# Kernel tuning notes

Measured on AMD Instinct MI355X. Metric: run time of the kernel, lower is better.

Reference implementation:

```python
import jax, jax.numpy as jnp
import numpy as np

N_NODES = 100000


def _deg_norm(idx, n):
    # inverse-sqrt degree, zero-degree nodes -> 0 (DGL norm='both' convention)
    deg = jax.ops.segment_sum(jnp.ones(idx.shape, jnp.float32), idx, num_segments=n)
    return jnp.where(deg > 0, jax.lax.rsqrt(jnp.maximum(deg, 1.0)), 0.0)


def graph_conv(x, src, dst, W, b, n):
    # symmetric normalization: D_out^{-1/2} on src, D_in^{-1/2} on dst
    norm_src = _deg_norm(src, n)  # [N]
    norm_dst = _deg_norm(dst, n)  # [N]
    h = (x * norm_src[:, None]) @ W          # apply weight first (in >= out)
    msg = h[src]                              # gather [E, out]
    agg = jax.ops.segment_sum(msg, dst, num_segments=n)  # scatter-add [N, out]
    return agg * norm_dst[:, None] + b


def setup_inputs() -> dict:
    key = jax.random.key(0)
    ks = jax.random.split(key, 6)
    x = jax.random.normal(ks[0], (N_NODES, 128), dtype=jnp.float32)
    edge_index = jax.random.randint(ks[1], (2, 1600000), 0, N_NODES, dtype=jnp.int64)
    W1 = jax.random.normal(ks[2], (128, 64), dtype=jnp.float32) * (1.0 / np.sqrt(128))
    b1 = jnp.zeros((64,), jnp.float32)
    W2 = jax.random.normal(ks[3], (64, 32), dtype=jnp.float32) * (1.0 / np.sqrt(64))
    b2 = jnp.zeros((32,), jnp.float32)
    Wl = jax.random.normal(ks[4], (32, 1), dtype=jnp.float32) * (1.0 / np.sqrt(32))
    bl = jnp.zeros((1,), jnp.float32)
    return {"x": x, "edge_index": edge_index, "W1": W1, "b1": b1,
            "W2": W2, "b2": b2, "Wl": Wl, "bl": bl}


def reference(x, edge_index, W1, b1, W2, b2, Wl, bl):
    src, dst = edge_index[0], edge_index[1]
    n = x.shape[0]
    h = graph_conv(x, src, dst, W1, b1, n)
    h = jax.nn.relu(h)
    # dropout(p=0.5) is identity at inference
    h = graph_conv(h, src, dst, W2, b2, n)
    return h @ Wl + bl  # [N, 1]
```

## Files before the change

### kernel.cpp

```cpp
#include <hip/hip_runtime.h>
#include <hip/hip_fp16.h>


#define WAVE 64
#define NRANGE 8
#define NQUAD 2
#define CB 1024

typedef _Float16 f16x8 __attribute__((ext_vector_type(8)));
typedef float f32x4 __attribute__((ext_vector_type(4)));

__global__ __launch_bounds__(256) void k_hist(const int* __restrict__ srcArr,
                                              const int* __restrict__ dstArr,
                                              unsigned* __restrict__ partial_s,
                                              unsigned* __restrict__ partial_d,
                                              int E, int B, int C, int chunkE) {
    extern __shared__ unsigned hist[];
    const int q = blockIdx.x & (NQUAD - 1);
    const int c = blockIdx.x >> 1;
    const int lo = q * 4 * B;
    const int* nodes = blockIdx.y ? dstArr : srcArr;
    unsigned* partial = blockIdx.y ? partial_d : partial_s;

    for (int b = threadIdx.x; b < B; b += 256) hist[b] = 0u;
    __syncthreads();

    const int beg = c * chunkE, end = min(beg + chunkE, E);
    const int n4 = (end - beg) >> 2;
    const int4* p = (const int4*)(nodes + beg);
    for (int j = threadIdx.x; j < n4; j += 256) {
        int4 v = p[j];
#pragma unroll
        for (int k = 0; k < 4; ++k) {
            int a = (&v.x)[k] - lo;
            if ((unsigned)a < (unsigned)(4 * B)) {
                int h2 = (a >= 2 * B);
                int r2 = a - (h2 ? 2 * B : 0);
                int h1 = (r2 >= B);
                int bin = r2 - (h1 ? B : 0);
                atomicAdd(&hist[bin], 1u << (((h2 << 1) | h1) << 3));
            }
        }
    }
    for (int j = beg + (n4 << 2) + threadIdx.x; j < end; j += 256) {
        int a = nodes[j] - lo;
        if ((unsigned)a < (unsigned)(4 * B)) {
            int h2 = (a >= 2 * B);
            int r2 = a - (h2 ? 2 * B : 0);
            int h1 = (r2 >= B);
            int bin = r2 - (h1 ? B : 0);
            atomicAdd(&hist[bin], 1u << (((h2 << 1) | h1) << 3));
        }
    }
    __syncthreads();
    unsigned* outp = partial + (size_t)(q * C + c) * B;
    for (int b = threadIdx.x; b < B; b += 256) outp[b] = hist[b];
}

__global__ __launch_bounds__(256) void k_reduce_norm(const unsigned* __restrict__ partial_s,
                                                     unsigned* __restrict__ partial_d,
                                                     float* __restrict__ norm_s,
                                                     float* __restrict__ norm_d,
                                                     unsigned* __restrict__ deg_d,
                                                     int N, int B, int C) {
    int t = blockIdx.x * 256 + threadIdx.x;
    if (t >= NQUAD * B) return;
    int q = t / B, b = t - q * B;
    size_t base = (size_t)(q * C) * B + b;
    unsigned ds = 0;
    for (int c = 0; c < C; ++c) ds += partial_s[base + (size_t)c * B];
    unsigned run = 0;
    for (int c = 0; c < C; ++c) {
        size_t ix = base + (size_t)c * B;
        unsigned v = partial_d[ix];
        partial_d[ix] = run;
        run += v;
    }
#pragma unroll
    for (int j = 0; j < 4; ++j) {
        int n = q * 4 * B + j * B + b;
        if (n < N) {
            unsigned d0 = (ds >> (8 * j)) & 0xffu;
            unsigned d1 = (run >> (8 * j)) & 0xffu;
            deg_d[n] = d1;
            norm_s[n] = d0 ? rsqrtf((float)d0) : 0.0f;
            norm_d[n] = d1 ? rsqrtf((float)d1) : 0.0f;
        }
    }
}

__global__ __launch_bounds__(256) void k_prep(const float* __restrict__ W1,
                                              const float* __restrict__ W2,
                                              const float* __restrict__ b2,
                                              const float* __restrict__ Wl,
                                              const float* __restrict__ bl,
                                              _Float16* __restrict__ wt,
                                              float* __restrict__ w2l,
                                              float* __restrict__ c0) {
    int t = threadIdx.x;
    for (int i = 0; i < 32; ++i) {
        int e = i * 256 + t;
        int k = e >> 6, n = e & 63;
        wt[n * 128 + k] = (_Float16)W1[e];
    }
    if (t < 64) {
        float acc = 0.f;
#pragma unroll
        for (int j = 0; j < 32; ++j) acc += W2[t * 32 + j] * Wl[j];
        w2l[t] = acc;
    }
    if (t == 0) {
        float s = 0.f;
#pragma unroll
        for (int j = 0; j < 32; ++j) s += b2[j] * Wl[j];
        *c0 = s + bl[0];
    }
}

__global__ __launch_bounds__(256) void k_blocksum(const unsigned* __restrict__ deg,
                                                  unsigned* __restrict__ partial, int N) {
    __shared__ unsigned sw[4];
    int i = blockIdx.x * 256 + threadIdx.x;
    unsigned v = (i < N) ? deg[i] : 0u;
#pragma unroll
    for (int off = 32; off; off >>= 1) v += __shfl_xor((int)v, off);
    if ((threadIdx.x & 63) == 0) sw[threadIdx.x >> 6] = v;
    __syncthreads();
    if (threadIdx.x == 0) partial[blockIdx.x] = sw[0] + sw[1] + sw[2] + sw[3];
}

__global__ __launch_bounds__(512) void k_scanpartial(const unsigned* __restrict__ partial,
                                                     unsigned* __restrict__ blockoff,
                                                     unsigned* __restrict__ offsets,
                                                     int nb, int N) {
    __shared__ unsigned s[512];
    int t = threadIdx.x;
    unsigned v = (t < nb) ? partial[t] : 0u;
    s[t] = v;
    __syncthreads();
    for (int off = 1; off < 512; off <<= 1) {
        unsigned a = (t >= off) ? s[t - off] : 0u;
        __syncthreads();
        s[t] += a;
        __syncthreads();
    }
    if (t < nb) blockoff[t] = s[t] - v;
    if (t == nb - 1) offsets[N] = s[t];
}

__global__ __launch_bounds__(256) void k_offsets(const unsigned* __restrict__ deg,
                                                 const unsigned* __restrict__ blockoff,
                                                 unsigned* __restrict__ offsets, int N) {
    __shared__ unsigned s[256];
    int t = threadIdx.x;
    int i = blockIdx.x * 256 + t;
    unsigned v = (i < N) ? deg[i] : 0u;
    s[t] = v;
    __syncthreads();
    for (int off = 1; off < 256; off <<= 1) {
        unsigned a = (t >= off) ? s[t - off] : 0u;
        __syncthreads();
        s[t] += a;
        __syncthreads();
    }
    if (i < N) offsets[i] = blockoff[blockIdx.x] + s[t] - v;
}

__global__ __launch_bounds__(256) void k_cnt(const int* __restrict__ dst,
                                             unsigned* __restrict__ cnt,
                                             int E, int B, int chunkEb) {
    __shared__ unsigned lc[NRANGE];
    if (threadIdx.x < NRANGE) lc[threadIdx.x] = 0u;
    __syncthreads();
    const int c = blockIdx.x;
    const int beg = c * chunkEb, end = min(beg + chunkEb, E);
    unsigned pc[NRANGE] = {};
    for (int i = beg + (int)threadIdx.x; i < end; i += 256) {
        int r = dst[i] / B;
#pragma unroll
        for (int rr = 0; rr < NRANGE; ++rr) pc[rr] += (r == rr);
    }
#pragma unroll
    for (int rr = 0; rr < NRANGE; ++rr) {
        unsigned v = pc[rr];
#pragma unroll
        for (int off = 32; off; off >>= 1) v += __shfl_xor((int)v, off);
        if ((threadIdx.x & 63) == 0 && v) atomicAdd(&lc[rr], v);
    }
    __syncthreads();
    if (threadIdx.x < NRANGE) cnt[threadIdx.x * CB + c] = lc[threadIdx.x];
}

__global__ __launch_bounds__(256) void k_scancnt2(const unsigned* __restrict__ cnt,
                                                  unsigned* __restrict__ segBase) {
    __shared__ unsigned s[256];
    const int t = threadIdx.x;
    const int PER = (NRANGE * CB) / 256;
    unsigned loc[PER];
    unsigned sum = 0;
#pragma unroll
    for (int j = 0; j < PER; ++j) { loc[j] = sum; sum += cnt[t * PER + j]; }
    s[t] = sum;
    __syncthreads();
    for (int off = 1; off < 256; off <<= 1) {
        unsigned a = (t >= off) ? s[t - off] : 0u;
        __syncthreads();
        s[t] += a;
        __syncthreads();
    }
    unsigned base = s[t] - sum;
#pragma unroll
    for (int j = 0; j < PER; ++j) segBase[t * PER + j] = base + loc[j];
    if (t == 255) segBase[NRANGE * CB] = s[255];
}

__global__ __launch_bounds__(256) void k_bucket(const int* __restrict__ src,
                                                const int* __restrict__ dst,
                                                const unsigned* __restrict__ segBase,
                                                uint2* __restrict__ ebuf,
                                                int E, int B, int chunkEb) {
    __shared__ unsigned lcnt[NRANGE];
    const int c = blockIdx.x;
    const int lane = threadIdx.x & 63;
    if (threadIdx.x < NRANGE) lcnt[threadIdx.x] = 0u;
    __syncthreads();

    unsigned sb[NRANGE];
#pragma unroll
    for (int r = 0; r < NRANGE; ++r) sb[r] = segBase[r * CB + c];

    const int beg = c * chunkEb, end = min(beg + chunkEb, E);
    for (int i = beg + (int)threadIdx.x; i < end; i += 256) {
        int d = dst[i];
        int s = src[i];
        int r = d / B;
#pragma unroll
        for (int rr = 0; rr < NRANGE; ++rr) {
            unsigned long long m = __ballot(r == rr);
            if (m) {
                int leader = __ffsll((long long)m) - 1;
                unsigned base = 0;
                if (lane == leader) base = atomicAdd(&lcnt[rr], (unsigned)__popcll(m));
                base = (unsigned)__shfl((int)base, leader);
                if (r == rr) {
                    unsigned before = (unsigned)__popcll(m & ((1ull << lane) - 1ull));
                    ebuf[sb[rr] + base + before] = make_uint2((unsigned)s, (unsigned)d);
                }
            }
        }
    }
}

__global__ __launch_bounds__(256) void k_fill2(const uint2* __restrict__ ebuf,
                                               const unsigned* __restrict__ segBase,
                                               const unsigned* __restrict__ offsets,
                                               const unsigned* __restrict__ rel,
                                               unsigned* __restrict__ csr,
                                               int N, int B, int C, int RB) {
    extern __shared__ unsigned curs[];
    const int r = blockIdx.x & (NRANGE - 1);
    const int ch = blockIdx.x >> 3;
    const int lo = r * B;
    const int bins = min(B, N - lo);
    const int sh = (r & 3) << 3;
    const unsigned* relp = rel + (size_t)((r >> 2) * C + ch) * B;
    for (int b = threadIdx.x; b < bins; b += 256)
        curs[b] = offsets[lo + b] + ((relp[b] >> sh) & 0xffu);
    __syncthreads();

    const unsigned s0 = segBase[r * CB + ch * RB];
    const unsigned s1 = segBase[r * CB + ch * RB + RB];
    for (unsigned i = s0 + threadIdx.x; i < s1; i += 256) {
        uint2 e = ebuf[i];
        int a = (int)e.y - lo;
        if ((unsigned)a < (unsigned)bins)
            csr[atomicAdd(&curs[a], 1u)] = e.x;
    }
}

__global__ __launch_bounds__(256) void k_gemm1(const float* __restrict__ x,
                                               const _Float16* __restrict__ wt,
                                               const float* __restrict__ norm_s,
                                               __half* __restrict__ h1h, int N) {
    __shared__ __align__(16) _Float16 xs[64 * 128];
    const int tid = threadIdx.x, lane = tid & 63, wv = tid >> 6;
    const int r0 = blockIdx.x * 64;

    f16x8 bf[4][4];
#pragma unroll
    for (int kt = 0; kt < 4; ++kt)
#pragma unroll
        for (int nt = 0; nt < 4; ++nt)
            bf[kt][nt] = *(const f16x8*)&wt[(nt * 16 + (lane & 15)) * 128 +
                                            kt * 32 + (lane >> 4) * 8];

#pragma unroll
    for (int it = 0; it < 8; ++it) {
        int e = it * 256 + tid;
        int r = e >> 5, c = e & 31;
        int row = r0 + r;
        float4 v = (row < N) ? ((const float4*)x)[(size_t)row * 32 + c]
                             : make_float4(0.f, 0.f, 0.f, 0.f);
        __half2 lo2 = __floats2half2_rn(v.x, v.y);
        __half2 hi2 = __floats2half2_rn(v.z, v.w);
        uint2 pk;
        pk.x = *(unsigned*)&lo2;
        pk.y = *(unsigned*)&hi2;
        int byte = r * 256 + c * 8;
        byte ^= (r & 7) << 4;
        *(uint2*)((char*)xs + byte) = pk;
    }
    __syncthreads();

    f32x4 acc[4] = {};
    const int rloc = wv * 16 + (lane & 15);
#pragma unroll
    for (int kt = 0; kt < 4; ++kt) {
        int byte = rloc * 256 + (kt * 32 + (lane >> 4) * 8) * 2;
        byte ^= (rloc & 7) << 4;
        f16x8 af = *(const f16x8*)((char*)xs + byte);
#pragma unroll
        for (int nt = 0; nt < 4; ++nt)
            acc[nt] = __builtin_amdgcn_mfma_f32_16x16x32_f16(af, bf[kt][nt], acc[nt], 0, 0, 0);
    }

#pragma unroll
    for (int j = 0; j < 4; ++j) {
        int row = r0 + wv * 16 + (lane >> 4) * 4 + j;
        if (row < N) {
            float ns = norm_s[row];
#pragma unroll
            for (int nt = 0; nt < 4; ++nt)
                h1h[(size_t)row * 64 + nt * 16 + (lane & 15)] =
                    __float2half(acc[nt][j] * ns);
        }
    }
}

__global__ __launch_bounds__(256) void k_agg_rdot(const unsigned* __restrict__ offsets,
                                                  const unsigned* __restrict__ csr,
                                                  const __half* __restrict__ h1h,
                                                  const float* __restrict__ norm_s,
                                                  const float* __restrict__ norm_d,
                                                  const float* __restrict__ b1,
                                                  const float* __restrict__ w2l,
                                                  float* __restrict__ s_node, int N) {
    const int lane = threadIdx.x & 63;
    const int slot = lane >> 4;
    const int p = lane & 15;
    const int v = (blockIdx.x * 256 + threadIdx.x) >> 6;
    if (v >= N) return;
    const unsigned beg = offsets[v], end = offsets[v + 1];

    float a0 = 0.f, a1 = 0.f, a2 = 0.f, a3 = 0.f;
#define GATHER(sreg) { \
        uint2 u = *(const uint2*)&h1h[(size_t)(sreg) * 64 + 4 * p]; \
        float2 f0 = __half22float2(*(__half2*)&u.x); \
        float2 f1 = __half22float2(*(__half2*)&u.y); \
        a0 += f0.x; a1 += f0.y; a2 += f1.x; a3 += f1.y; }

    for (unsigned base = beg; base < end; base += WAVE) {
        const int n = (int)min((unsigned)WAVE, end - base);
        int sv = (lane < n) ? (int)csr[base + lane] : 0;
        int i = 0;
        for (; i + 32 <= n; i += 32) {
            int s0 = __shfl(sv, i + 0 + slot);
            int s1 = __shfl(sv, i + 4 + slot);
            int s2 = __shfl(sv, i + 8 + slot);
            int s3 = __shfl(sv, i + 12 + slot);
            int s4 = __shfl(sv, i + 16 + slot);
            int s5 = __shfl(sv, i + 20 + slot);
            int s6 = __shfl(sv, i + 24 + slot);
            int s7 = __shfl(sv, i + 28 + slot);
            GATHER(s0); GATHER(s1); GATHER(s2); GATHER(s3);
            GATHER(s4); GATHER(s5); GATHER(s6); GATHER(s7);
        }
        for (; i + 16 <= n; i += 16) {
            int s0 = __shfl(sv, i + 0 + slot);
            int s1 = __shfl(sv, i + 4 + slot);
            int s2 = __shfl(sv, i + 8 + slot);
            int s3 = __shfl(sv, i + 12 + slot);
            GATHER(s0); GATHER(s1); GATHER(s2); GATHER(s3);
        }
        for (; i < n; i += 4) {
            int e = i + slot;
            int s = __shfl(sv, min(e, n - 1));
            if (e < n) GATHER(s);
        }
    }
#undef GATHER
    a0 += __shfl_xor(a0, 16); a0 += __shfl_xor(a0, 32);
    a1 += __shfl_xor(a1, 16); a1 += __shfl_xor(a1, 32);
    a2 += __shfl_xor(a2, 16); a2 += __shfl_xor(a2, 32);
    a3 += __shfl_xor(a3, 16); a3 += __shfl_xor(a3, 32);

    float nd = norm_d[v];
    float4 bq = *(const float4*)&b1[4 * p];
    float4 wq = *(const float4*)&w2l[4 * p];
    float t = fmaxf(fmaf(a0, nd, bq.x), 0.f) * wq.x
            + fmaxf(fmaf(a1, nd, bq.y), 0.f) * wq.y
            + fmaxf(fmaf(a2, nd, bq.z), 0.f) * wq.z
            + fmaxf(fmaf(a3, nd, bq.w), 0.f) * wq.w;
#pragma unroll
    for (int off = 8; off; off >>= 1) t += __shfl_xor(t, off);
    if (lane == 0) s_node[v] = t * norm_s[v];
}

__global__ __launch_bounds__(256) void k_out(const unsigned* __restrict__ offsets,
                                             const unsigned* __restrict__ csr,
                                             const float* __restrict__ s_node,
                                             const float* __restrict__ norm_d,
                                             const float* __restrict__ c0,
                                             float* __restrict__ out, int N) {
    int v = blockIdx.x * 256 + threadIdx.x;
    if (v >= N) return;
    unsigned beg = offsets[v], end = offsets[v + 1];
    float sum = 0.f;
    unsigned j = beg;
    for (; j + 4 <= end; j += 4) {
        float a = s_node[csr[j + 0]], b = s_node[csr[j + 1]];
        float c = s_node[csr[j + 2]], d = s_node[csr[j + 3]];
        sum += a + b + c + d;
    }
    for (; j < end; ++j) sum += s_node[csr[j]];
    out[v] = fmaf(sum, norm_d[v], *c0);
}

extern "C" void kernel_launch(void* const* d_in, const int* in_sizes, int n_in,
                              void* d_out, int out_size, void* d_ws, size_t ws_size,
                              hipStream_t stream) {
    const float* x  = (const float*)d_in[0];
    const int*   ei = (const int*)d_in[1];
    const float* W1 = (const float*)d_in[2];
    const float* b1 = (const float*)d_in[3];
    const float* W2 = (const float*)d_in[4];
    const float* b2 = (const float*)d_in[5];
    const float* Wl = (const float*)d_in[6];
    const float* bl = (const float*)d_in[7];

    const int N = in_sizes[0] / 128;
    const int E = in_sizes[1] / 2;
    const int* src = ei;
    const int* dst = ei + E;
    const int NB = (N + 255) / 256;
    const int B = (N + NRANGE - 1) / NRANGE;

    size_t baseBytes = 0;
    {
        auto pad = [](size_t b) { return (b + 255) & ~(size_t)255; };
        baseBytes = pad((size_t)N * 4) * 3 + pad((size_t)(N + 1) * 4) +
                    pad((size_t)NB * 4) * 2 + pad((size_t)N * 64 * 2) +
                    pad((size_t)E * 4) + pad((size_t)N * 4) + pad(64 * 4) + pad(4) +
                    pad(64 * 128 * 2) + pad((size_t)E * 8) +
                    pad((size_t)(NRANGE * CB + 1) * 4) * 2;
    }
    int C = 64;
    while (C > 4 && baseBytes + 2ull * NQUAD * C * B * 4ull > ws_size) C >>= 1;
    const int chunkEb = (E + CB - 1) / CB;
    const int RB = CB / C;
    const int chunkE = chunkEb * RB;

    char* w = (char*)d_ws;
    auto alloc = [&](size_t bytes) -> void* {
        void* r = (void*)w;
        w += (bytes + 255) & ~(size_t)255;
        return r;
    };
    float*    norm_s    = (float*)alloc((size_t)N * 4);
    float*    norm_d    = (float*)alloc((size_t)N * 4);
    unsigned* deg_d     = (unsigned*)alloc((size_t)N * 4);
    unsigned* offsets   = (unsigned*)alloc((size_t)(N + 1) * 4);
    unsigned* partial   = (unsigned*)alloc((size_t)NB * 4);
    unsigned* blockoff  = (unsigned*)alloc((size_t)NB * 4);
    __half*   h1h       = (__half*)alloc((size_t)N * 64 * 2);
    unsigned* csr       = (unsigned*)alloc((size_t)E * 4);
    float*    s_node    = (float*)alloc((size_t)N * 4);
    float*    w2l       = (float*)alloc(64 * 4);
    float*    c0        = (float*)alloc(4);
    _Float16* wt        = (_Float16*)alloc(64 * 128 * 2);
    uint2*    ebuf      = (uint2*)alloc((size_t)E * 8);
    unsigned* cnt       = (unsigned*)alloc((size_t)(NRANGE * CB + 1) * 4);
    unsigned* segBase   = (unsigned*)alloc((size_t)(NRANGE * CB + 1) * 4);
    unsigned* partial_s = (unsigned*)alloc((size_t)NQUAD * C * B * 4);
    unsigned* partial_d = (unsigned*)alloc((size_t)NQUAD * C * B * 4);

    float* out = (float*)d_out;
    const size_t ldsB = (size_t)B * 4;

    k_cnt<<<CB, 256, 0, stream>>>(dst, cnt, E, B, chunkEb);
    k_scancnt2<<<1, 256, 0, stream>>>(cnt, segBase);
    k_bucket<<<CB, 256, 0, stream>>>(src, dst, segBase, ebuf, E, B, chunkEb);

    k_hist<<<dim3(NQUAD * C, 2), 256, ldsB, stream>>>(src, dst, partial_s, partial_d,
                                                      E, B, C, chunkE);
    k_prep<<<1, 256, 0, stream>>>(W1, W2, b2, Wl, bl, wt, w2l, c0);

    k_reduce_norm<<<(NQUAD * B + 255) / 256, 256, 0, stream>>>(partial_s, partial_d,
                                                               norm_s, norm_d,
                                                               deg_d, N, B, C);
    k_blocksum<<<NB, 256, 0, stream>>>(deg_d, partial, N);
    k_scanpartial<<<1, 512, 0, stream>>>(partial, blockoff, offsets, NB, N);
    k_offsets<<<NB, 256, 0, stream>>>(deg_d, blockoff, offsets, N);

    k_fill2<<<NRANGE * C, 256, ldsB, stream>>>(ebuf, segBase, offsets, partial_d,
                                               csr, N, B, C, RB);

    k_gemm1<<<(N + 63) / 64, 256, 0, stream>>>(x, wt, norm_s, h1h, N);

    k_agg_rdot<<<(N + 3) / 4, 256, 0, stream>>>(offsets, csr, h1h, norm_s, norm_d,
                                                b1, w2l, s_node, N);
    k_out<<<NB, 256, 0, stream>>>(offsets, csr, s_node, norm_d, c0, out, N);
}
```

Baseline: 195.7 us.

## Replace global offset scan with wave scan plus per-range atomic slot allocation

Removes the three-kernel exclusive scan (blocksum, scanpartial, offsets) by computing CSR offsets inside the reduce-norm kernel. Each wave does a shuffle scan and claims space with an atomicAdd on a per-range cursor in a padded slotted CSR buffer, and consumers use offset plus degree instead of offsets[v+1]. It also folds the weight prep kernel into an extra block of the count kernel and fixes the hist chunk count at a compile-time 32. The trade-off is a non-deterministic CSR order, slot overflow if any range exceeds E/8+16384 edges, and a fixed chunk count that no longer adapts to workspace size.

```diff
diff --git a/kernel.cpp b/kernel.cpp
--- a/kernel.cpp
+++ b/kernel.cpp
@@ -6,15 +6,97 @@
 #define NRANGE 8
 #define NQUAD 2
 #define CB 1024
+#define CHK 32
+#define RB (CB / CHK)
 
 typedef _Float16 f16x8 __attribute__((ext_vector_type(8)));
 typedef float f32x4 __attribute__((ext_vector_type(4)));
+
+__global__ __launch_bounds__(256) void k_cnt(const int* __restrict__ dst,
+                                             unsigned* __restrict__ cnt,
+                                             int E, int B, int chunkEb,
+                                             const float* __restrict__ W1,
+                                             const float* __restrict__ W2,
+                                             const float* __restrict__ b2,
+                                             const float* __restrict__ Wl,
+                                             const float* __restrict__ bl,
+                                             _Float16* __restrict__ wt,
+                                             float* __restrict__ w2l,
+                                             float* __restrict__ c0) {
+    if (blockIdx.x == CB) {
+        int t = threadIdx.x;
+        for (int i = 0; i < 32; ++i) {
+            int e = i * 256 + t;
+            int k = e >> 6, n = e & 63;
+            wt[n * 128 + k] = (_Float16)W1[e];
+        }
+        if (t < 64) {
+            float acc = 0.f;
+#pragma unroll
+            for (int j = 0; j < 32; ++j) acc += W2[t * 32 + j] * Wl[j];
+            w2l[t] = acc;
+        }
+        if (t == 0) {
+            float s = 0.f;
+#pragma unroll
+            for (int j = 0; j < 32; ++j) s += b2[j] * Wl[j];
+            *c0 = s + bl[0];
+        }
+        return;
+    }
+    __shared__ unsigned lc[NRANGE];
+    if (threadIdx.x < NRANGE) lc[threadIdx.x] = 0u;
+    __syncthreads();
+    const int c = blockIdx.x;
+    const int beg = c * chunkEb, end = min(beg + chunkEb, E);
+    unsigned pc[NRANGE] = {};
+    for (int i = beg + (int)threadIdx.x; i < end; i += 256) {
+        int r = dst[i] / B;
+#pragma unroll
+        for (int rr = 0; rr < NRANGE; ++rr) pc[rr] += (r == rr);
+    }
+#pragma unroll
+    for (int rr = 0; rr < NRANGE; ++rr) {
+        unsigned v = pc[rr];
+#pragma unroll
+        for (int off = 32; off; off >>= 1) v += __shfl_xor((int)v, off);
+        if ((threadIdx.x & 63) == 0 && v) atomicAdd(&lc[rr], v);
+    }
+    __syncthreads();
+    if (threadIdx.x < NRANGE) cnt[threadIdx.x * CB + c] = lc[threadIdx.x];
+}
+
+__global__ __launch_bounds__(256) void k_scancnt2(const unsigned* __restrict__ cnt,
+                                                  unsigned* __restrict__ segBase,
+                                                  unsigned* __restrict__ rangeCur,
+                                                  int SLOT) {
+    __shared__ unsigned s[256];
+    const int t = threadIdx.x;
+    const int PER = (NRANGE * CB) / 256;
+    unsigned loc[PER];
+    unsigned sum = 0;
+#pragma unroll
+    for (int j = 0; j < PER; ++j) { loc[j] = sum; sum += cnt[t * PER + j]; }
+    s[t] = sum;
+    __syncthreads();
+    for (int off = 1; off < 256; off <<= 1) {
+        unsigned a = (t >= off) ? s[t - off] : 0u;
+        __syncthreads();
+        s[t] += a;
+        __syncthreads();
+    }
+    unsigned base = s[t] - sum;
+#pragma unroll
+    for (int j = 0; j < PER; ++j) segBase[t * PER + j] = base + loc[j];
+    if (t == 255) segBase[NRANGE * CB] = s[255];
+    if (t < NRANGE) rangeCur[t] = (unsigned)(t * SLOT);
+}
 
 __global__ __launch_bounds__(256) void k_hist(const int* __restrict__ srcArr,
                                               const int* __restrict__ dstArr,
                                               unsigned* __restrict__ partial_s,
                                               unsigned* __restrict__ partial_d,
-                                              int E, int B, int C, int chunkE) {
+                                              int E, int B, int chunkE) {
     extern __shared__ unsigned hist[];
     const int q = blockIdx.x & (NQUAD - 1);
     const int c = blockIdx.x >> 1;
@@ -53,165 +135,8 @@
         }
     }
     __syncthreads();
-    unsigned* outp = partial + (size_t)(q * C + c) * B;
+    unsigned* outp = partial + (size_t)(q * CHK + c) * B;
     for (int b = threadIdx.x; b < B; b += 256) outp[b] = hist[b];
-}
-
-__global__ __launch_bounds__(256) void k_reduce_norm(const unsigned* __restrict__ partial_s,
-                                                     unsigned* __restrict__ partial_d,
-                                                     float* __restrict__ norm_s,
-                                                     float* __restrict__ norm_d,
-                                                     unsigned* __restrict__ deg_d,
-                                                     int N, int B, int C) {
-    int t = blockIdx.x * 256 + threadIdx.x;
-    if (t >= NQUAD * B) return;
-    int q = t / B, b = t - q * B;
-    size_t base = (size_t)(q * C) * B + b;
-    unsigned ds = 0;
-    for (int c = 0; c < C; ++c) ds += partial_s[base + (size_t)c * B];
-    unsigned run = 0;
-    for (int c = 0; c < C; ++c) {
-        size_t ix = base + (size_t)c * B;
-        unsigned v = partial_d[ix];
-        partial_d[ix] = run;
-        run += v;
-    }
-#pragma unroll
-    for (int j = 0; j < 4; ++j) {
-        int n = q * 4 * B + j * B + b;
-        if (n < N) {
-            unsigned d0 = (ds >> (8 * j)) & 0xffu;
-            unsigned d1 = (run >> (8 * j)) & 0xffu;
-            deg_d[n] = d1;
-            norm_s[n] = d0 ? rsqrtf((float)d0) : 0.0f;
-            norm_d[n] = d1 ? rsqrtf((float)d1) : 0.0f;
-        }
-    }
-}
-
-__global__ __launch_bounds__(256) void k_prep(const float* __restrict__ W1,
-                                              const float* __restrict__ W2,
-                                              const float* __restrict__ b2,
-                                              const float* __restrict__ Wl,
-                                              const float* __restrict__ bl,
-                                              _Float16* __restrict__ wt,
-                                              float* __restrict__ w2l,
-                                              float* __restrict__ c0) {
-    int t = threadIdx.x;
-    for (int i = 0; i < 32; ++i) {
-        int e = i * 256 + t;
-        int k = e >> 6, n = e & 63;
-        wt[n * 128 + k] = (_Float16)W1[e];
-    }
-    if (t < 64) {
-        float acc = 0.f;
-#pragma unroll
-        for (int j = 0; j < 32; ++j) acc += W2[t * 32 + j] * Wl[j];
-        w2l[t] = acc;
-    }
-    if (t == 0) {
-        float s = 0.f;
-#pragma unroll
-        for (int j = 0; j < 32; ++j) s += b2[j] * Wl[j];
-        *c0 = s + bl[0];
-    }
-}
-
-__global__ __launch_bounds__(256) void k_blocksum(const unsigned* __restrict__ deg,
-                                                  unsigned* __restrict__ partial, int N) {
-    __shared__ unsigned sw[4];
-    int i = blockIdx.x * 256 + threadIdx.x;
-    unsigned v = (i < N) ? deg[i] : 0u;
-#pragma unroll
-    for (int off = 32; off; off >>= 1) v += __shfl_xor((int)v, off);
-    if ((threadIdx.x & 63) == 0) sw[threadIdx.x >> 6] = v;
-    __syncthreads();
-    if (threadIdx.x == 0) partial[blockIdx.x] = sw[0] + sw[1] + sw[2] + sw[3];
-}
-
-__global__ __launch_bounds__(512) void k_scanpartial(const unsigned* __restrict__ partial,
-                                                     unsigned* __restrict__ blockoff,
-                                                     unsigned* __restrict__ offsets,
-                                                     int nb, int N) {
-    __shared__ unsigned s[512];
-    int t = threadIdx.x;
-    unsigned v = (t < nb) ? partial[t] : 0u;
-    s[t] = v;
-    __syncthreads();
-    for (int off = 1; off < 512; off <<= 1) {
-        unsigned a = (t >= off) ? s[t - off] : 0u;
-        __syncthreads();
-        s[t] += a;
-        __syncthreads();
-    }
-    if (t < nb) blockoff[t] = s[t] - v;
-    if (t == nb - 1) offsets[N] = s[t];
-}
-
-__global__ __launch_bounds__(256) void k_offsets(const unsigned* __restrict__ deg,
-                                                 const unsigned* __restrict__ blockoff,
-                                                 unsigned* __restrict__ offsets, int N) {
-    __shared__ unsigned s[256];
-    int t = threadIdx.x;
-    int i = blockIdx.x * 256 + t;
-    unsigned v = (i < N) ? deg[i] : 0u;
-    s[t] = v;
-    __syncthreads();
-    for (int off = 1; off < 256; off <<= 1) {
-        unsigned a = (t >= off) ? s[t - off] : 0u;
-        __syncthreads();
-        s[t] += a;
-        __syncthreads();
-    }
-    if (i < N) offsets[i] = blockoff[blockIdx.x] + s[t] - v;
-}
-
-__global__ __launch_bounds__(256) void k_cnt(const int* __restrict__ dst,
-                                             unsigned* __restrict__ cnt,
-                                             int E, int B, int chunkEb) {
-    __shared__ unsigned lc[NRANGE];
-    if (threadIdx.x < NRANGE) lc[threadIdx.x] = 0u;
-    __syncthreads();
-    const int c = blockIdx.x;
-    const int beg = c * chunkEb, end = min(beg + chunkEb, E);
-    unsigned pc[NRANGE] = {};
-    for (int i = beg + (int)threadIdx.x; i < end; i += 256) {
-        int r = dst[i] / B;
-#pragma unroll
-        for (int rr = 0; rr < NRANGE; ++rr) pc[rr] += (r == rr);
-    }
-#pragma unroll
-    for (int rr = 0; rr < NRANGE; ++rr) {
-        unsigned v = pc[rr];
-#pragma unroll
-        for (int off = 32; off; off >>= 1) v += __shfl_xor((int)v, off);
-        if ((threadIdx.x & 63) == 0 && v) atomicAdd(&lc[rr], v);
-    }
-    __syncthreads();
-    if (threadIdx.x < NRANGE) cnt[threadIdx.x * CB + c] = lc[threadIdx.x];
-}
-
-__global__ __launch_bounds__(256) void k_scancnt2(const unsigned* __restrict__ cnt,
-                                                  unsigned* __restrict__ segBase) {
-    __shared__ unsigned s[256];
-    const int t = threadIdx.x;
-    const int PER = (NRANGE * CB) / 256;
-    unsigned loc[PER];
-    unsigned sum = 0;
-#pragma unroll
-    for (int j = 0; j < PER; ++j) { loc[j] = sum; sum += cnt[t * PER + j]; }
-    s[t] = sum;
-    __syncthreads();
-    for (int off = 1; off < 256; off <<= 1) {
-        unsigned a = (t >= off) ? s[t - off] : 0u;
-        __syncthreads();
-        s[t] += a;
-        __syncthreads();
-    }
-    unsigned base = s[t] - sum;
-#pragma unroll
-    for (int j = 0; j < PER; ++j) segBase[t * PER + j] = base + loc[j];
-    if (t == 255) segBase[NRANGE * CB] = s[255];
 }
 
 __global__ __launch_bounds__(256) void k_bucket(const int* __restrict__ src,
@@ -251,19 +176,71 @@
     }
 }
 
+__global__ __launch_bounds__(256) void k_reduce_norm(const unsigned* __restrict__ partial_s,
+                                                     unsigned* __restrict__ partial_d,
+                                                     float* __restrict__ norm_s,
+                                                     float* __restrict__ norm_d,
+                                                     unsigned* __restrict__ deg_d,
+                                                     unsigned* __restrict__ offsets,
+                                                     unsigned* __restrict__ rangeCur,
+                                                     int N, int B, int Bpad) {
+    int t = blockIdx.x * 256 + threadIdx.x;
+    int lane = threadIdx.x & 63;
+    int q = t / Bpad, b = t - q * Bpad;
+    bool valid = (q < NQUAD) && (b < B);
+    unsigned ds = 0, run = 0;
+    if (valid) {
+        size_t base = (size_t)(q * CHK) * B + b;
+        for (int c = 0; c < CHK; ++c) ds += partial_s[base + (size_t)c * B];
+        unsigned acc = 0;
+        for (int c = 0; c < CHK; ++c) {
+            size_t ix = base + (size_t)c * B;
+            unsigned v = partial_d[ix];
+            partial_d[ix] = acc;
+            acc += v;
+        }
+        run = acc;
+    }
+#pragma unroll
+    for (int j = 0; j < 4; ++j) {
+        unsigned d1 = valid ? ((run >> (8 * j)) & 0xffu) : 0u;
+        unsigned p = d1;
+#pragma unroll
+        for (int off = 1; off < 64; off <<= 1) {
+            unsigned o = (unsigned)__shfl_up((int)p, off);
+            if (lane >= off) p += o;
+        }
+        unsigned tot = (unsigned)__shfl((int)p, 63);
+        int r = q * 4 + j;
+        unsigned wbase = 0;
+        if (lane == 63 && tot) wbase = atomicAdd(&rangeCur[r], tot);
+        wbase = (unsigned)__shfl((int)wbase, 63);
+        if (valid) {
+            int n = q * 4 * B + j * B + b;
+            if (n < N) {
+                unsigned d0 = (ds >> (8 * j)) & 0xffu;
+                deg_d[n] = d1;
+                norm_s[n] = d0 ? rsqrtf((float)d0) : 0.0f;
+                norm_d[n] = d1 ? rsqrtf((float)d1) : 0.0f;
+                offsets[n] = wbase + (p - d1);
+            }
+        }
+    }
+}
+
 __global__ __launch_bounds__(256) void k_fill2(const uint2* __restrict__ ebuf,
                                                const unsigned* __restrict__ segBase,
                                                const unsigned* __restrict__ offsets,
                                                const unsigned* __restrict__ rel,
                                                unsigned* __restrict__ csr,
-                                               int N, int B, int C, int RB) {
+                                               int N, int B) {
     extern __shared__ unsigned curs[];
     const int r = blockIdx.x & (NRANGE - 1);
     const int ch = blockIdx.x >> 3;
     const int lo = r * B;
     const int bins = min(B, N - lo);
     const int sh = (r & 3) << 3;
-    const unsigned* relp = rel + (size_t)((r >> 2) * C + ch) * B;
+    const unsigned* relp = rel + (size_t)((r >> 2) * CHK + ch) * B;
     for (int b = threadIdx.x; b < bins; b += 256)
         curs[b] = offsets[lo + b] + ((relp[b] >> sh) & 0xffu);
     __syncthreads();
@@ -338,6 +315,7 @@
 }
 
 __global__ __launch_bounds__(256) void k_agg_rdot(const unsigned* __restrict__ offsets,
+                                                  const unsigned* __restrict__ deg_d,
                                                   const unsigned* __restrict__ csr,
                                                   const __half* __restrict__ h1h,
                                                   const float* __restrict__ norm_s,
@@ -350,7 +328,8 @@
     const int p = lane & 15;
     const int v = (blockIdx.x * 256 + threadIdx.x) >> 6;
     if (v >= N) return;
-    const unsigned beg = offsets[v], end = offsets[v + 1];
+    const unsigned beg = offsets[v];
+    const unsigned end = beg + deg_d[v];
 
     float a0 = 0.f, a1 = 0.f, a2 = 0.f, a3 = 0.f;
 #define GATHER(sreg) { \
@@ -407,6 +386,7 @@
 }
 
 __global__ __launch_bounds__(256) void k_out(const unsigned* __restrict__ offsets,
+                                             const unsigned* __restrict__ deg_d,
                                              const unsigned* __restrict__ csr,
                                              const float* __restrict__ s_node,
                                              const float* __restrict__ norm_d,
@@ -414,13 +394,13 @@
                                              float* __restrict__ out, int N) {
     int v = blockIdx.x * 256 + threadIdx.x;
     if (v >= N) return;
-    unsigned beg = offsets[v], end = offsets[v + 1];
+    unsigned beg = offsets[v], end = beg + deg_d[v];
     float sum = 0.f;
     unsigned j = beg;
     for (; j + 4 <= end; j += 4) {
         float a = s_node[csr[j + 0]], b = s_node[csr[j + 1]];
         float c = s_node[csr[j + 2]], d = s_node[csr[j + 3]];
-        sum += a + b + c + d;
+        sum += (a + b) + (c + d);
     }
     for (; j < end; ++j) sum += s_node[csr[j]];
     out[v] = fmaf(sum, norm_d[v], *c0);
@@ -444,20 +424,9 @@
     const int* dst = ei + E;
     const int NB = (N + 255) / 256;
     const int B = (N + NRANGE - 1) / NRANGE;
-
-    size_t baseBytes = 0;
-    {
-        auto pad = [](size_t b) { return (b + 255) & ~(size_t)255; };
-        baseBytes = pad((size_t)N * 4) * 3 + pad((size_t)(N + 1) * 4) +
-                    pad((size_t)NB * 4) * 2 + pad((size_t)N * 64 * 2) +
-                    pad((size_t)E * 4) + pad((size_t)N * 4) + pad(64 * 4) + pad(4) +
-                    pad(64 * 128 * 2) + pad((size_t)E * 8) +
-                    pad((size_t)(NRANGE * CB + 1) * 4) * 2;
-    }
-    int C = 64;
-    while (C > 4 && baseBytes + 2ull * NQUAD * C * B * 4ull > ws_size) C >>= 1;
+    const int Bpad = ((B + 63) / 64) * 64;
+    const int SLOT = E / NRANGE + 16384;
     const int chunkEb = (E + CB - 1) / CB;
-    const int RB = CB / C;
     const int chunkE = chunkEb * RB;
 
     char* w = (char*)d_ws;
@@ -469,11 +438,9 @@
     float*    norm_s    = (float*)alloc((size_t)N * 4);
     float*    norm_d    = (float*)alloc((size_t)N * 4);
     unsigned* deg_d     = (unsigned*)alloc((size_t)N * 4);
-    unsigned* offsets   = (unsigned*)alloc((size_t)(N + 1) * 4);
-    unsigned* partial   = (unsigned*)alloc((size_t)NB * 4);
-    unsigned* blockoff  = (unsigned*)alloc((size_t)NB * 4);
+    unsigned* offsets   = (unsigned*)alloc((size_t)N * 4);
     __half*   h1h       = (__half*)alloc((size_t)N * 64 * 2);
-    unsigned* csr       = (unsigned*)alloc((size_t)E * 4);
+    unsigned* csr       = (unsigned*)alloc((size_t)NRANGE * SLOT * 4);
     float*    s_node    = (float*)alloc((size_t)N * 4);
     float*    w2l       = (float*)alloc(64 * 4);
     float*    c0        = (float*)alloc(4);
@@ -481,33 +448,31 @@
     uint2*    ebuf      = (uint2*)alloc((size_t)E * 8);
     unsigned* cnt       = (unsigned*)alloc((size_t)(NRANGE * CB + 1) * 4);
     unsigned* segBase   = (unsigned*)alloc((size_t)(NRANGE * CB + 1) * 4);
-    unsigned* partial_s = (unsigned*)alloc((size_t)NQUAD * C * B * 4);
-    unsigned* partial_d = (unsigned*)alloc((size_t)NQUAD * C * B * 4);
+    unsigned* rangeCur  = (unsigned*)alloc(NRANGE * 4);
+    unsigned* partial_s = (unsigned*)alloc((size_t)NQUAD * CHK * B * 4);
+    unsigned* partial_d = (unsigned*)alloc((size_t)NQUAD * CHK * B * 4);
 
     float* out = (float*)d_out;
     const size_t ldsB = (size_t)B * 4;
 
-    k_cnt<<<CB, 256, 0, stream>>>(dst, cnt, E, B, chunkEb);
-    k_scancnt2<<<1, 256, 0, stream>>>(cnt, segBase);
+    k_cnt<<<CB + 1, 256, 0, stream>>>(dst, cnt, E, B, chunkEb,
+                                      W1, W2, b2, Wl, bl, wt, w2l, c0);
+    k_scancnt2<<<1, 256, 0, stream>>>(cnt, segBase, rangeCur, SLOT);
+    k_hist<<<dim3(NQUAD * CHK, 2), 256, ldsB, stream>>>(src, dst, partial_s,
+                                                        partial_d, E, B, chunkE);
     k_bucket<<<CB, 256, 0, stream>>>(src, dst, segBase, ebuf, E, B, chunkEb);
 
-    k_hist<<<dim3(NQUAD * C, 2), 256, ldsB, stream>>>(src, dst, partial_s, partial_d,
-                                                      E, B, C, chunkE);
-    k_prep<<<1, 256, 0, stream>>>(W1, W2, b2, Wl, bl, wt, w2l, c0);
-
-    k_reduce_norm<<<(NQUAD * B + 255) / 256, 256, 0, stream>>>(partial_s, partial_d,
-                                                               norm_s, norm_d,
-                                                               deg_d, N, B, C);
-    k_blocksum<<<NB, 256, 0, stream>>>(deg_d, partial, N);
-    k_scanpartial<<<1, 512, 0, stream>>>(partial, blockoff, offsets, NB, N);
-    k_offsets<<<NB, 256, 0, stream>>>(deg_d, blockoff, offsets, N);
-
-    k_fill2<<<NRANGE * C, 256, ldsB, stream>>>(ebuf, segBase, offsets, partial_d,
-                                               csr, N, B, C, RB);
+    k_reduce_norm<<<(NQUAD * Bpad + 255) / 256, 256, 0, stream>>>(
+        partial_s, partial_d, norm_s, norm_d, deg_d, offsets, rangeCur,
+        N, B, Bpad);
 
     k_gemm1<<<(N + 63) / 64, 256, 0, stream>>>(x, wt, norm_s, h1h, N);
 
-    k_agg_rdot<<<(N + 3) / 4, 256, 0, stream>>>(offsets, csr, h1h, norm_s, norm_d,
-                                                b1, w2l, s_node, N);
-    k_out<<<NB, 256, 0, stream>>>(offsets, csr, s_node, norm_d, c0, out, N);
-}
+    k_fill2<<<NRANGE * CHK, 256, ldsB, stream>>>(ebuf, segBase, offsets,
+                                                 partial_d, csr, N, B);
+
+    k_agg_rdot<<<(N + 3) / 4, 256, 0, stream>>>(offsets, deg_d, csr, h1h,
+                                                norm_s, norm_d, b1, w2l,
+                                                s_node, N);
+    k_out<<<NB, 256, 0, stream>>>(offsets, deg_d, csr, s_node, norm_d, c0, out, N);
+}
```

Result: faster. 188.5 us (-3.7%).
